# Kernel optimization log

Measured on AMD Instinct MI355X. Metric: run time of the kernel, lower is better.

## Reference

```python
import jax, jax.numpy as jnp
import numpy as np

RADIUS = 0.2
NSAMPLE = 32
MLP_CH = [67, 64, 64, 128]  # in = 3 (rel xyz) + 64 (features)


def _ball_query(xyz, radius, nsample):
    """xyz: (B,N,3) centers == points. Returns (B,N,nsample) int32 neighbor idx."""
    sq = jnp.sum(xyz * xyz, axis=-1)  # (B,N)
    d2 = sq[:, :, None] + sq[:, None, :] - 2.0 * jnp.einsum('bnd,bmd->bnm', xyz, xyz)
    N = xyz.shape[1]
    in_ball = d2 < radius * radius
    cand = jnp.where(in_ball, jnp.arange(N, dtype=jnp.int32)[None, None, :], N)
    idx = jnp.sort(cand, axis=-1)[..., :nsample]  # first nsample hits (by index)
    # pad slots with the first valid neighbor (self-point always within radius)
    return jnp.where(idx == N, idx[..., :1], idx)


def setup_inputs() -> dict:
    key = jax.random.key(0)
    ks = jax.random.split(key, 8)
    B, N, C = 4, 4096, 64
    d = {
        'xyz': jax.random.uniform(ks[0], (B, N, 3), jnp.float32),
        'features': jax.random.normal(ks[1], (B, C, N), jnp.float32),
    }
    for i in range(3):
        cin, cout = MLP_CH[i], MLP_CH[i + 1]
        d[f'W{i+1}'] = jax.random.normal(ks[2 + i], (cout, cin), jnp.float32) / np.float32(np.sqrt(cin))
        d[f's{i+1}'] = jnp.ones((cout,), jnp.float32)   # folded BN scale
        d[f't{i+1}'] = jnp.zeros((cout,), jnp.float32)  # folded BN shift
    return d


def reference(xyz, features, W1, s1, t1, W2, s2, t2, W3, s3, t3):
    idx = _ball_query(xyz, RADIUS, NSAMPLE)              # (B,N,ns) int
    B = xyz.shape[0]
    bidx = jnp.arange(B)[:, None, None]
    grouped_xyz = xyz[bidx, idx] - xyz[:, :, None, :]    # (B,N,ns,3) relative coords
    grouped_feat = jnp.transpose(features, (0, 2, 1))[bidx, idx]  # (B,N,ns,C)
    h = jnp.concatenate([grouped_xyz, grouped_feat], axis=-1)     # (B,N,ns,3+C)
    for W, s, t in ((W1, s1, t1), (W2, s2, t2), (W3, s3, t3)):
        # shared 1x1 conv (pointwise linear) + folded BN + ReLU
        h = jax.nn.relu(jnp.einsum('bnkc,oc->bnko', h, W) * s + t)
    pooled = jnp.max(h, axis=2)                          # max over nsample -> (B,N,Cout)
    new_features = jnp.transpose(pooled, (0, 2, 1))      # (B,Cout,npoint)
    return xyz, new_features
```

## Files before the change

### kernel.cpp

```cpp
#include <hip/hip_runtime.h>
#include <cstdint>

#define NPT   4096
#define NBAT  4
#define NS    32
#define R2C   0.04f

#define OFF_XYZ4 0
#define OFF_F1S  65536
#define OFF_PT   1114112
#define OFF_WX   3211264
#define OFF_W1T  3211520
#define OFF_IDX  3227904
#define OFF_W2PH 3752192
#define OFF_W2PL 3754240
#define OFF_W3PH 3756288
#define OFF_W3PL 3760384

typedef __attribute__((ext_vector_type(8))) short bf16x8;
typedef __attribute__((ext_vector_type(4))) float f32x4;

__device__ __host__ inline unsigned short f2bf(float x) {
  unsigned u = __builtin_bit_cast(unsigned, x);
  return (unsigned short)((u + 0x7FFFu + ((u >> 16) & 1u)) >> 16);
}
__device__ inline float bf2f(unsigned short h) {
  return __uint_as_float(((unsigned)h) << 16);
}

#define SWZ(row, us) (((row) << 6) + ((us) ^ (((row) & 7) << 3)))

__global__ __launch_bounds__(256) void k_prep(
    const float* __restrict__ W1, const float* __restrict__ s1,
    const float* __restrict__ W2, const float* __restrict__ s2,
    const float* __restrict__ W3, const float* __restrict__ s3,
    float* __restrict__ ws) {
  int i = blockIdx.x * 256 + threadIdx.x;
  if (i < 256) { int c = i >> 2, d = i & 3;
    ws[OFF_WX + i] = (d < 3) ? W1[c * 67 + d] * s1[c] : 0.f; }
  if (i < 4096) { int c = i >> 6, co = i & 63;
    ws[OFF_W1T + c * 64 + co] = W1[co * 67 + 3 + c] * s1[co]; }
  if (i < 4096) { int o = i >> 6, c = i & 63;
    float x = W2[o * 64 + c] * s2[o];
    unsigned short h = f2bf(x), lo = f2bf(x - bf2f(h));
    ((unsigned short*)(ws + OFF_W2PH))[i] = h;
    ((unsigned short*)(ws + OFF_W2PL))[i] = lo; }
  if (i < 8192) { int o = i >> 6, c = i & 63;
    float x = W3[o * 64 + c] * s3[o];
    unsigned short h = f2bf(x), lo = f2bf(x - bf2f(h));
    ((unsigned short*)(ws + OFF_W3PH))[i] = h;
    ((unsigned short*)(ws + OFF_W3PL))[i] = lo; }
}

__global__ __launch_bounds__(256) void k_xyz4(const float* __restrict__ xyz,
                                              float* __restrict__ ws) {
  int i = blockIdx.x * 256 + threadIdx.x;
  float x = xyz[i * 3], y = xyz[i * 3 + 1], z = xyz[i * 3 + 2];
  float sq = __fadd_rn(__fadd_rn(__fmul_rn(x, x), __fmul_rn(y, y)), __fmul_rn(z, z));
  ((float4*)(ws + OFF_XYZ4))[i] = make_float4(x, y, z, sq);
}

__global__ __launch_bounds__(256, 2) void k_bq(const float* __restrict__ ws,
                                               int* __restrict__ idxo) {
  __shared__ float4 sxb[NPT / 2];
  int tid = threadIdx.x, lane = tid & 63;
  int center = blockIdx.x * 4 + (tid >> 6);
  int b = center >> 12, n = center & 4095;
  const float4* xb = (const float4*)(ws + OFF_XYZ4) + b * NPT;
  float4 cp = xb[n];
  unsigned long long lmask = (1ull << lane) - 1ull;
  int cnt = 0, first = 0;
#pragma unroll 1
  for (int half = 0; half < 2; ++half) {
    __syncthreads();
    for (int i = tid; i < NPT / 2; i += 256) sxb[i] = xb[half * (NPT / 2) + i];
    __syncthreads();
    if (cnt >= NS) continue;
    float4 p = sxb[lane];
#pragma unroll 1
    for (int ch = 0; ch < 32; ++ch) {
      float4 pn = sxb[((ch + 1) & 31) * 64 + lane];
      float dot = __fadd_rn(__fadd_rn(__fmul_rn(p.x, cp.x), __fmul_rn(p.y, cp.y)),
                            __fmul_rn(p.z, cp.z));
      float d2 = __fsub_rn(__fadd_rn(cp.w, p.w), __fmul_rn(2.f, dot));
      bool hit = d2 <= R2C;
      unsigned long long mk = __ballot(hit);
      int m = half * (NPT / 2) + ch * 64 + lane;
      if (mk) {
        if (cnt == 0) first = m - lane + __builtin_ctzll(mk);
        int pos = cnt + (int)__popcll(mk & lmask);
        if (hit && pos < NS) idxo[center * NS + pos] = m;
        cnt += (int)__popcll(mk);
        if (cnt >= NS) break;
      }
      p = pn;
    }
  }
  if (cnt < NS && lane >= cnt && lane < NS) idxo[center * NS + lane] = first;
}

__global__ __launch_bounds__(256, 4) void k_f1(
    const float* __restrict__ feat, const float* __restrict__ t1,
    const float* __restrict__ w1t, float* __restrict__ f1out) {
  int gid = blockIdx.x * 256 + threadIdx.x;
  int chunk = gid >> 14, ml = gid & 16383;
  int b = ml >> 12, m = ml & 4095;
  float acc[16];
#pragma unroll
  for (int j = 0; j < 16; ++j) acc[j] = t1[chunk * 16 + j];
#pragma unroll
  for (int c = 0; c < 64; ++c) {
    float f = feat[(b * 64 + c) * NPT + m];
#pragma unroll
    for (int j = 0; j < 16; ++j)
      acc[j] = fmaf(w1t[c * 64 + chunk * 16 + j], f, acc[j]);
  }
  float* o = f1out + (size_t)(b * NPT + m) * 64 + chunk * 16;
#pragma unroll
  for (int j = 0; j < 4; ++j)
    ((float4*)o)[j] = make_float4(acc[4 * j], acc[4 * j + 1], acc[4 * j + 2], acc[4 * j + 3]);
}

__global__ __launch_bounds__(256) void k_mlp(
    const float* __restrict__ ws_c, const int* __restrict__ idxp,
    const float* __restrict__ t2, const float* __restrict__ t3,
    float* __restrict__ pooledT) {
  __shared__ unsigned short A1hi[4096], A1lo[4096], A2hi[4096], A2lo[4096];
  int tid = threadIdx.x, blk = blockIdx.x;
  int l = tid & 63, w = tid >> 6;
  int col = l & 15, kg = l >> 4;

  {
    int si = tid >> 2, q = tid & 3;
    int center = blk * 2 + (si >> 5);
    int b = center >> 12, n = center & 4095;
    int m = idxp[center * NS + (si & 31)];
    const float4* xb = (const float4*)(ws_c + OFF_XYZ4) + b * NPT;
    float4 cp = xb[n], np = xb[m];
    float rx = np.x - cp.x, ry = np.y - cp.y, rz = np.z - cp.z;
    const float4* f1p = (const float4*)(ws_c + OFF_F1S) + (size_t)(b * NPT + m) * 16 + q * 4;
    const float* wx = ws_c + OFF_WX + q * 64;
    unsigned short hi[16], lo[16];
#pragma unroll
    for (int j = 0; j < 4; ++j) {
      float4 fq = f1p[j];
      float hv[4] = {fq.x, fq.y, fq.z, fq.w};
#pragma unroll
      for (int e = 0; e < 4; ++e) {
        int cc = 4 * j + e;
        float t = fmaf(wx[cc * 4 + 2], rz, fmaf(wx[cc * 4 + 1], ry, fmaf(wx[cc * 4], rx, hv[e])));
        t = fmaxf(t, 0.f);
        hi[cc] = f2bf(t);
        lo[cc] = f2bf(t - bf2f(hi[cc]));
      }
    }
#pragma unroll
    for (int h8 = 0; h8 < 2; ++h8) {
      bf16x8 vh, vl;
#pragma unroll
      for (int e = 0; e < 8; ++e) { vh[e] = (short)hi[h8 * 8 + e]; vl[e] = (short)lo[h8 * 8 + e]; }
      *(bf16x8*)&A1hi[SWZ(si, q * 16 + 8 * h8)] = vh;
      *(bf16x8*)&A1lo[SWZ(si, q * 16 + 8 * h8)] = vl;
    }
  }
  __syncthreads();

  {
    const unsigned short* w2ph = (const unsigned short*)(ws_c + OFF_W2PH);
    const unsigned short* w2pl = (const unsigned short*)(ws_c + OFF_W2PL);
    int o = 16 * w + col;
    bf16x8 bh[2], bl[2];
#pragma unroll
    for (int ks = 0; ks < 2; ++ks) {
      bh[ks] = *(const bf16x8*)&w2ph[o * 64 + 32 * ks + 8 * kg];
      bl[ks] = *(const bf16x8*)&w2pl[o * 64 + 32 * ks + 8 * kg];
    }
    float bias = t2[o];
#pragma unroll
    for (int mt = 0; mt < 4; ++mt) {
      int ar = 16 * mt + col;
      f32x4 acc = {bias, bias, bias, bias};
#pragma unroll
      for (int ks = 0; ks < 2; ++ks) {
        bf16x8 ah = *(const bf16x8*)&A1hi[SWZ(ar, 32 * ks + 8 * kg)];
        bf16x8 al = *(const bf16x8*)&A1lo[SWZ(ar, 32 * ks + 8 * kg)];
        acc = __builtin_amdgcn_mfma_f32_16x16x32_bf16(ah, bh[ks], acc, 0, 0, 0);
        acc = __builtin_amdgcn_mfma_f32_16x16x32_bf16(ah, bl[ks], acc, 0, 0, 0);
        acc = __builtin_amdgcn_mfma_f32_16x16x32_bf16(al, bh[ks], acc, 0, 0, 0);
      }
#pragma unroll
      for (int r = 0; r < 4; ++r) {
        float v = fmaxf(acc[r], 0.f);
        unsigned short h = f2bf(v), l2 = f2bf(v - bf2f(h));
        int row2 = 16 * mt + 4 * kg + r;
        A2hi[SWZ(row2, 16 * w + col)] = h;
        A2lo[SWZ(row2, 16 * w + col)] = l2;
      }
    }
  }
  __syncthreads();

  {
    const unsigned short* w3ph = (const unsigned short*)(ws_c + OFF_W3PH);
    const unsigned short* w3pl = (const unsigned short*)(ws_c + OFF_W3PL);
    bf16x8 bh[2][2], bl[2][2];
    float bias3[2];
#pragma unroll
    for (int nts = 0; nts < 2; ++nts) {
      int o = 16 * (w + 4 * nts) + col;
      bias3[nts] = t3[o];
#pragma unroll
      for (int ks = 0; ks < 2; ++ks) {
        bh[nts][ks] = *(const bf16x8*)&w3ph[o * 64 + 32 * ks + 8 * kg];
        bl[nts][ks] = *(const bf16x8*)&w3pl[o * 64 + 32 * ks + 8 * kg];
      }
    }
    float p00 = 0.f, p01 = 0.f, p10 = 0.f, p11 = 0.f;
#pragma unroll
    for (int mt = 0; mt < 4; ++mt) {
      int ar = 16 * mt + col;
      bf16x8 ah[2], al[2];
#pragma unroll
      for (int ks = 0; ks < 2; ++ks) {
        ah[ks] = *(const bf16x8*)&A2hi[SWZ(ar, 32 * ks + 8 * kg)];
        al[ks] = *(const bf16x8*)&A2lo[SWZ(ar, 32 * ks + 8 * kg)];
      }
#pragma unroll
      for (int nts = 0; nts < 2; ++nts) {
        f32x4 acc = {bias3[nts], bias3[nts], bias3[nts], bias3[nts]};
#pragma unroll
        for (int ks = 0; ks < 2; ++ks) {
          acc = __builtin_amdgcn_mfma_f32_16x16x32_bf16(ah[ks], bh[nts][ks], acc, 0, 0, 0);
          acc = __builtin_amdgcn_mfma_f32_16x16x32_bf16(ah[ks], bl[nts][ks], acc, 0, 0, 0);
          acc = __builtin_amdgcn_mfma_f32_16x16x32_bf16(al[ks], bh[nts][ks], acc, 0, 0, 0);
        }
        float m4 = fmaxf(fmaxf(fmaxf(acc[0], acc[1]), fmaxf(acc[2], acc[3])), 0.f);
        if (mt < 2) { if (nts == 0) p00 = fmaxf(p00, m4); else p01 = fmaxf(p01, m4); }
        else        { if (nts == 0) p10 = fmaxf(p10, m4); else p11 = fmaxf(p11, m4); }
      }
    }
    p00 = fmaxf(p00, __shfl_xor(p00, 16)); p00 = fmaxf(p00, __shfl_xor(p00, 32));
    p01 = fmaxf(p01, __shfl_xor(p01, 16)); p01 = fmaxf(p01, __shfl_xor(p01, 32));
    p10 = fmaxf(p10, __shfl_xor(p10, 16)); p10 = fmaxf(p10, __shfl_xor(p10, 32));
    p11 = fmaxf(p11, __shfl_xor(p11, 16)); p11 = fmaxf(p11, __shfl_xor(p11, 32));
    int c2s = (l >> 5) & 1, ns = (l >> 4) & 1;
    float va = c2s ? p10 : p00, vb = c2s ? p11 : p01;
    float val = ns ? vb : va;
    int ch = 16 * (w + 4 * ns) + col;
    pooledT[(size_t)(blk * 2 + c2s) * 128 + ch] = val;
  }
}

__global__ __launch_bounds__(256) void k_tr(const float* __restrict__ pooledT,
                                            float* __restrict__ out) {
  __shared__ float tile[64][65];
  int b = blockIdx.z;
  int o0 = blockIdx.y * 64, n0 = blockIdx.x * 64;
  int tx = threadIdx.x & 63, ty = threadIdx.x >> 6;
#pragma unroll
  for (int j = 0; j < 16; ++j) {
    int r = j * 4 + ty;
    tile[r][tx] = pooledT[(size_t)(b * NPT + n0 + r) * 128 + o0 + tx];
  }
  __syncthreads();
#pragma unroll
  for (int j = 0; j < 16; ++j) {
    int r = j * 4 + ty;
    out[(size_t)(b * 128 + o0 + r) * NPT + n0 + tx] = tile[tx][r];
  }
}

extern "C" void kernel_launch(void* const* d_in, const int* in_sizes, int n_in,
                              void* d_out, int out_size, void* d_ws, size_t ws_size,
                              hipStream_t stream) {
  const float* xyz = (const float*)d_in[0];
  const float* feat = (const float*)d_in[1];
  const float* W1 = (const float*)d_in[2];
  const float* s1 = (const float*)d_in[3];
  const float* t1 = (const float*)d_in[4];
  const float* W2 = (const float*)d_in[5];
  const float* s2 = (const float*)d_in[6];
  const float* t2 = (const float*)d_in[7];
  const float* W3 = (const float*)d_in[8];
  const float* s3 = (const float*)d_in[9];
  const float* t3 = (const float*)d_in[10];
  float* ws = (float*)d_ws;
  int* idxp = (int*)(ws + OFF_IDX);
  float* out = (float*)d_out;

  hipMemcpyAsync(out, xyz, (size_t)NBAT * NPT * 3 * sizeof(float),
                 hipMemcpyDeviceToDevice, stream);

  k_prep<<<32, 256, 0, stream>>>(W1, s1, W2, s2, W3, s3, ws);
  k_xyz4<<<64, 256, 0, stream>>>(xyz, ws);
  k_bq<<<4096, 256, 0, stream>>>(ws, idxp);
  k_f1<<<256, 256, 0, stream>>>(feat, t1, ws + OFF_W1T, ws + OFF_F1S);
  k_mlp<<<8192, 256, 0, stream>>>(ws, idxp, t2, t3, ws + OFF_PT);
  k_tr<<<dim3(64, 2, 4), 256, 0, stream>>>(ws + OFF_PT, out + NBAT * NPT * 3);
}
```

Before: 247.4 us.

## Reuse one LDS buffer across MLP layers and split MFMA accumulation chains

The fused MLP kernel now shares one hi/lo LDS buffer pair between layer-2 input and layer-3 input, halving shared memory per block. An extra barrier lets layer-2 results sit in registers before overwriting the buffer. Weight fragments for both layers are loaded up front, and each output tile uses two independent accumulators instead of one serial chain of six MFMAs. The aim is higher occupancy and shorter MFMA dependency chains, at the cost of more registers and an added barrier.

```diff
diff --git a/kernel.cpp b/kernel.cpp
--- a/kernel.cpp
+++ b/kernel.cpp
@@ -125,10 +125,34 @@
     const float* __restrict__ ws_c, const int* __restrict__ idxp,
     const float* __restrict__ t2, const float* __restrict__ t3,
     float* __restrict__ pooledT) {
-  __shared__ unsigned short A1hi[4096], A1lo[4096], A2hi[4096], A2lo[4096];
+  __shared__ __align__(16) unsigned short Hhi[4096], Hlo[4096];
   int tid = threadIdx.x, blk = blockIdx.x;
   int l = tid & 63, w = tid >> 6;
   int col = l & 15, kg = l >> 4;
+
+  const unsigned short* w2ph = (const unsigned short*)(ws_c + OFF_W2PH);
+  const unsigned short* w2pl = (const unsigned short*)(ws_c + OFF_W2PL);
+  const unsigned short* w3ph = (const unsigned short*)(ws_c + OFF_W3PH);
+  const unsigned short* w3pl = (const unsigned short*)(ws_c + OFF_W3PL);
+  int o2 = 16 * w + col;
+  bf16x8 b2h[2], b2l[2], b3h[2][2], b3l[2][2];
+#pragma unroll
+  for (int ks = 0; ks < 2; ++ks) {
+    b2h[ks] = *(const bf16x8*)&w2ph[o2 * 64 + 32 * ks + 8 * kg];
+    b2l[ks] = *(const bf16x8*)&w2pl[o2 * 64 + 32 * ks + 8 * kg];
+  }
+  float bias2 = t2[o2];
+  float bias3[2];
+#pragma unroll
+  for (int nts = 0; nts < 2; ++nts) {
+    int o3 = 16 * (w + 4 * nts) + col;
+    bias3[nts] = t3[o3];
+#pragma unroll
+    for (int ks = 0; ks < 2; ++ks) {
+      b3h[nts][ks] = *(const bf16x8*)&w3ph[o3 * 64 + 32 * ks + 8 * kg];
+      b3l[nts][ks] = *(const bf16x8*)&w3pl[o3 * 64 + 32 * ks + 8 * kg];
+    }
+  }
 
   {
     int si = tid >> 2, q = tid & 3;
@@ -159,62 +183,49 @@
       bf16x8 vh, vl;
 #pragma unroll
       for (int e = 0; e < 8; ++e) { vh[e] = (short)hi[h8 * 8 + e]; vl[e] = (short)lo[h8 * 8 + e]; }
-      *(bf16x8*)&A1hi[SWZ(si, q * 16 + 8 * h8)] = vh;
-      *(bf16x8*)&A1lo[SWZ(si, q * 16 + 8 * h8)] = vl;
+      *(bf16x8*)&Hhi[SWZ(si, q * 16 + 8 * h8)] = vh;
+      *(bf16x8*)&Hlo[SWZ(si, q * 16 + 8 * h8)] = vl;
     }
   }
   __syncthreads();
 
+  float dres[4][4];
+#pragma unroll
+  for (int mt = 0; mt < 4; ++mt) {
+    int ar = 16 * mt + col;
+    bf16x8 ah[2], al[2];
+#pragma unroll
+    for (int ks = 0; ks < 2; ++ks) {
+      ah[ks] = *(const bf16x8*)&Hhi[SWZ(ar, 32 * ks + 8 * kg)];
+      al[ks] = *(const bf16x8*)&Hlo[SWZ(ar, 32 * ks + 8 * kg)];
+    }
+    f32x4 accA = {bias2, bias2, bias2, bias2};
+    f32x4 accB = {0.f, 0.f, 0.f, 0.f};
+    accA = __builtin_amdgcn_mfma_f32_16x16x32_bf16(ah[0], b2h[0], accA, 0, 0, 0);
+    accB = __builtin_amdgcn_mfma_f32_16x16x32_bf16(ah[0], b2l[0], accB, 0, 0, 0);
+    accA = __builtin_amdgcn_mfma_f32_16x16x32_bf16(ah[1], b2h[1], accA, 0, 0, 0);
+    accB = __builtin_amdgcn_mfma_f32_16x16x32_bf16(ah[1], b2l[1], accB, 0, 0, 0);
+    accB = __builtin_amdgcn_mfma_f32_16x16x32_bf16(al[0], b2h[0], accB, 0, 0, 0);
+    accB = __builtin_amdgcn_mfma_f32_16x16x32_bf16(al[1], b2h[1], accB, 0, 0, 0);
+#pragma unroll
+    for (int r = 0; r < 4; ++r) dres[mt][r] = fmaxf(accA[r] + accB[r], 0.f);
+  }
+  __syncthreads();
+
+#pragma unroll
+  for (int mt = 0; mt < 4; ++mt) {
+#pragma unroll
+    for (int r = 0; r < 4; ++r) {
+      float v = dres[mt][r];
+      unsigned short h = f2bf(v), l2 = f2bf(v - bf2f(h));
+      int row2 = 16 * mt + 4 * kg + r;
+      Hhi[SWZ(row2, o2)] = h;
+      Hlo[SWZ(row2, o2)] = l2;
+    }
+  }
+  __syncthreads();
+
   {
-    const unsigned short* w2ph = (const unsigned short*)(ws_c + OFF_W2PH);
-    const unsigned short* w2pl = (const unsigned short*)(ws_c + OFF_W2PL);
-    int o = 16 * w + col;
-    bf16x8 bh[2], bl[2];
-#pragma unroll
-    for (int ks = 0; ks < 2; ++ks) {
-      bh[ks] = *(const bf16x8*)&w2ph[o * 64 + 32 * ks + 8 * kg];
-      bl[ks] = *(const bf16x8*)&w2pl[o * 64 + 32 * ks + 8 * kg];
-    }
-    float bias = t2[o];
-#pragma unroll
-    for (int mt = 0; mt < 4; ++mt) {
-      int ar = 16 * mt + col;
-      f32x4 acc = {bias, bias, bias, bias};
-#pragma unroll
-      for (int ks = 0; ks < 2; ++ks) {
-        bf16x8 ah = *(const bf16x8*)&A1hi[SWZ(ar, 32 * ks + 8 * kg)];
-        bf16x8 al = *(const bf16x8*)&A1lo[SWZ(ar, 32 * ks + 8 * kg)];
-        acc = __builtin_amdgcn_mfma_f32_16x16x32_bf16(ah, bh[ks], acc, 0, 0, 0);
-        acc = __builtin_amdgcn_mfma_f32_16x16x32_bf16(ah, bl[ks], acc, 0, 0, 0);
-        acc = __builtin_amdgcn_mfma_f32_16x16x32_bf16(al, bh[ks], acc, 0, 0, 0);
-      }
-#pragma unroll
-      for (int r = 0; r < 4; ++r) {
-        float v = fmaxf(acc[r], 0.f);
-        unsigned short h = f2bf(v), l2 = f2bf(v - bf2f(h));
-        int row2 = 16 * mt + 4 * kg + r;
-        A2hi[SWZ(row2, 16 * w + col)] = h;
-        A2lo[SWZ(row2, 16 * w + col)] = l2;
-      }
-    }
-  }
-  __syncthreads();
-
-  {
-    const unsigned short* w3ph = (const unsigned short*)(ws_c + OFF_W3PH);
-    const unsigned short* w3pl = (const unsigned short*)(ws_c + OFF_W3PL);
-    bf16x8 bh[2][2], bl[2][2];
-    float bias3[2];
-#pragma unroll
-    for (int nts = 0; nts < 2; ++nts) {
-      int o = 16 * (w + 4 * nts) + col;
-      bias3[nts] = t3[o];
-#pragma unroll
-      for (int ks = 0; ks < 2; ++ks) {
-        bh[nts][ks] = *(const bf16x8*)&w3ph[o * 64 + 32 * ks + 8 * kg];
-        bl[nts][ks] = *(const bf16x8*)&w3pl[o * 64 + 32 * ks + 8 * kg];
-      }
-    }
     float p00 = 0.f, p01 = 0.f, p10 = 0.f, p11 = 0.f;
 #pragma unroll
     for (int mt = 0; mt < 4; ++mt) {
@@ -222,19 +233,21 @@
       bf16x8 ah[2], al[2];
 #pragma unroll
       for (int ks = 0; ks < 2; ++ks) {
-        ah[ks] = *(const bf16x8*)&A2hi[SWZ(ar, 32 * ks + 8 * kg)];
-        al[ks] = *(const bf16x8*)&A2lo[SWZ(ar, 32 * ks + 8 * kg)];
+        ah[ks] = *(const bf16x8*)&Hhi[SWZ(ar, 32 * ks + 8 * kg)];
+        al[ks] = *(const bf16x8*)&Hlo[SWZ(ar, 32 * ks + 8 * kg)];
       }
 #pragma unroll
       for (int nts = 0; nts < 2; ++nts) {
-        f32x4 acc = {bias3[nts], bias3[nts], bias3[nts], bias3[nts]};
-#pragma unroll
-        for (int ks = 0; ks < 2; ++ks) {
-          acc = __builtin_amdgcn_mfma_f32_16x16x32_bf16(ah[ks], bh[nts][ks], acc, 0, 0, 0);
-          acc = __builtin_amdgcn_mfma_f32_16x16x32_bf16(ah[ks], bl[nts][ks], acc, 0, 0, 0);
-          acc = __builtin_amdgcn_mfma_f32_16x16x32_bf16(al[ks], bh[nts][ks], acc, 0, 0, 0);
-        }
-        float m4 = fmaxf(fmaxf(fmaxf(acc[0], acc[1]), fmaxf(acc[2], acc[3])), 0.f);
+        f32x4 accA = {bias3[nts], bias3[nts], bias3[nts], bias3[nts]};
+        f32x4 accB = {0.f, 0.f, 0.f, 0.f};
+        accA = __builtin_amdgcn_mfma_f32_16x16x32_bf16(ah[0], b3h[nts][0], accA, 0, 0, 0);
+        accB = __builtin_amdgcn_mfma_f32_16x16x32_bf16(ah[0], b3l[nts][0], accB, 0, 0, 0);
+        accA = __builtin_amdgcn_mfma_f32_16x16x32_bf16(ah[1], b3h[nts][1], accA, 0, 0, 0);
+        accB = __builtin_amdgcn_mfma_f32_16x16x32_bf16(ah[1], b3l[nts][1], accB, 0, 0, 0);
+        accB = __builtin_amdgcn_mfma_f32_16x16x32_bf16(al[0], b3h[nts][0], accB, 0, 0, 0);
+        accB = __builtin_amdgcn_mfma_f32_16x16x32_bf16(al[1], b3h[nts][1], accB, 0, 0, 0);
+        float m4 = fmaxf(fmaxf(fmaxf(accA[0] + accB[0], accA[1] + accB[1]),
+                               fmaxf(accA[2] + accB[2], accA[3] + accB[3])), 0.f);
         if (mt < 2) { if (nts == 0) p00 = fmaxf(p00, m4); else p01 = fmaxf(p01, m4); }
         else        { if (nts == 0) p10 = fmaxf(p10, m4); else p11 = fmaxf(p11, m4); }
       }
```

After: 247.1 us. No clear change (-0.1%).
